# Kernel tuning notes

Hardware: AMD Instinct MI355X
Metric: run time of the kernel (lower is better)

The kernel has to match this reference:

```python
import jax, jax.numpy as jnp
import numpy as np


def setup_inputs() -> dict:
    key = jax.random.key(0)
    k1, k2 = jax.random.split(key)
    qs = jax.random.normal(k1, (8, 4096, 1024), dtype=jnp.float32)      # [B, L, D]
    memory = jax.random.normal(k2, (512, 1024), dtype=jnp.float32)       # [M, D]
    return {"qs": qs, "memory": memory}


def reference(qs, memory):
    # s = qs @ memory.T  -> [B, L, M]; permute -> [B, M, L]
    s = jnp.einsum("bld,md->bml", qs, memory)
    # softmax over L (last dim after permute)
    v = jax.nn.softmax(s, axis=2)                 # [B, M, L]
    # r = v @ qs -> [B, M, D]
    r = jnp.einsum("bml,bld->bmd", v, qs)
    return (r, memory)
```

## Files before the change

### kernel.cpp

```cpp
#include <hip/hip_runtime.h>
#include <hip/hip_fp16.h>


#define B_ 8
#define L_ 4096
#define D_ 1024
#define M_ 512

typedef _Float16 halfT;
typedef _Float16 half8 __attribute__((ext_vector_type(8)));
typedef _Float16 half4_t __attribute__((ext_vector_type(4)));
typedef float f32x4 __attribute__((ext_vector_type(4)));

#define OFF_MEM16 0ull
#define SZ_MEM16  (512ull*1024*2)
#define OFF_QS16  (OFF_MEM16 + SZ_MEM16)
#define SZ_QS16   (8ull*4096*1024*2)
#define OFF_S     (OFF_QS16 + SZ_QS16)
#define SZ_S      (8ull*512*4096*4)
#define OFF_P16   (OFF_S + SZ_S)
#define SZ_P16    (8ull*512*4096*2)
#define OFF_INVL  (OFF_P16 + SZ_P16)
#define SZ_INVL   (8ull*512*4)
#define WS_NEED   (OFF_INVL + SZ_INVL)
#define OFF_RP    OFF_S

#define SWZ(n) ((((n)&7) ^ (((n)>>5)&7)))

__device__ __forceinline__ void gload_lds16(const halfT* g, halfT* l) {
  __builtin_amdgcn_global_load_lds(
      (const __attribute__((address_space(1))) unsigned int*)(const void*)g,
      (__attribute__((address_space(3))) unsigned int*)l, 16, 0, 0);
}

__global__ __launch_bounds__(256)
void prep_mem16(const float* __restrict__ mem, halfT* __restrict__ mem16) {
  int i8 = blockIdx.x*256 + threadIdx.x;
  int row = i8 >> 7, c = i8 & 127;
  int kt = c >> 3, g = c & 7;
  const float* src = mem + (size_t)i8*8;
  f32x4 x0 = *(const f32x4*)src;
  f32x4 x1 = *(const f32x4*)(src + 4);
  half8 h;
  #pragma unroll
  for (int j = 0; j < 4; ++j) { h[j] = (halfT)x0[j]; h[4+j] = (halfT)x1[j]; }
  *(half8*)&mem16[(size_t)row*1024 + kt*64 + ((g ^ (row & 7)) << 3)] = h;
}

__global__ __launch_bounds__(256)
void prep_qs16(const float* __restrict__ qs, halfT* __restrict__ q16) {
  size_t base = (size_t)blockIdx.x*256 + threadIdx.x;
  #pragma unroll
  for (int it = 0; it < 8; ++it) {
    size_t i8 = base + (size_t)it*524288;
    size_t row = i8 >> 7;
    int c = (int)(i8 & 127);
    int kt = c >> 3, g = c & 7;
    const float* src = qs + i8*8;
    f32x4 x0 = *(const f32x4*)src;
    f32x4 x1 = *(const f32x4*)(src + 4);
    half8 h;
    #pragma unroll
    for (int j = 0; j < 4; ++j) { h[j] = (halfT)x0[j]; h[4+j] = (halfT)x1[j]; }
    *(half8*)&q16[row*1024 + kt*64 + ((g ^ ((int)row & 7)) << 3)] = h;
  }
}

__global__ __launch_bounds__(512, 2)
void gemm_qk(const halfT* __restrict__ mem16, const halfT* __restrict__ qs16,
             float* __restrict__ S)
{
  __shared__ __attribute__((aligned(16))) halfT At[2][256*64];
  __shared__ __attribute__((aligned(16))) halfT Bt[2][256*64];

  int bid = blockIdx.x;
  int swz = (bid & 7)*32 + (bid >> 3);
  int b   = swz >> 5;
  int rem = swz & 31;
  int nt  = rem >> 1;
  int mt  = rem & 1;

  int tid = threadIdx.x;
  int w = tid >> 6, lane = tid & 63, lg = lane >> 4, li = lane & 15;
  int wm = w >> 2, wn = w & 3;
  int sl = li & 7;
  int rA = tid >> 3;
  int cA = (tid & 7)*8;

  const halfT* Ab = mem16 + (size_t)mt*256*1024;
  const halfT* Bb = qs16 + ((size_t)b*L_ + nt*256)*D_;

  f32x4 acc[8][4];
  #pragma unroll
  for (int i=0;i<8;++i)
    #pragma unroll
    for (int j=0;j<4;++j) acc[i][j] = (f32x4){0.f,0.f,0.f,0.f};

#define STAGE_QK(nb_, kt_)                                                     \
  do {                                                                         \
    const halfT* a0 = Ab + (size_t)(kt_)*64 + cA;                              \
    const halfT* b0 = Bb + (size_t)(kt_)*64 + cA;                              \
    _Pragma("unroll")                                                          \
    for (int j = 0; j < 4; ++j) {                                              \
      int r = rA + j*64;                                                       \
      gload_lds16(a0 + (size_t)r*1024, &At[nb_][(tid + j*512)*8]);             \
      gload_lds16(b0 + (size_t)r*1024, &Bt[nb_][(tid + j*512)*8]);             \
    }                                                                          \
  } while (0)

  STAGE_QK(0, 0);
  __syncthreads();

  int nb = 0;
  for (int kt = 0; kt < 16; ++kt) {
    if (kt + 1 < 16) STAGE_QK(nb ^ 1, kt + 1);
    #pragma unroll
    for (int ksub = 0; ksub < 2; ++ksub) {
      int gx = ((ksub*4 + lg) ^ sl) << 3;
      half8 Af[8], Bf[4];
      #pragma unroll
      for (int mf = 0; mf < 8; ++mf)
        Af[mf] = *(const half8*)&At[nb][(wm*128 + mf*16 + li)*64 + gx];
      #pragma unroll
      for (int nf = 0; nf < 4; ++nf)
        Bf[nf] = *(const half8*)&Bt[nb][(wn*64 + nf*16 + li)*64 + gx];
      #pragma unroll
      for (int mf = 0; mf < 8; ++mf)
        #pragma unroll
        for (int nf = 0; nf < 4; ++nf)
          acc[mf][nf] = __builtin_amdgcn_mfma_f32_16x16x32_f16(Af[mf], Bf[nf], acc[mf][nf], 0,0,0);
    }
    __syncthreads();
    nb ^= 1;
  }
#undef STAGE_QK

  float* Cb = S + (size_t)b*M_*L_;
  int colbase = nt*256 + wn*64;
  #pragma unroll
  for (int mf = 0; mf < 8; ++mf) {
    #pragma unroll
    for (int r = 0; r < 4; ++r) {
      int row = mt*256 + wm*128 + mf*16 + lg*4 + r;
      #pragma unroll
      for (int nf = 0; nf < 4; ++nf)
        Cb[(size_t)row*L_ + colbase + nf*16 + li] = acc[mf][nf][r];
    }
  }
}

__global__ __launch_bounds__(512, 2)
void gemm_pv(const halfT* __restrict__ P16, const halfT* __restrict__ qs16,
             float* __restrict__ rp)
{
  __shared__ __attribute__((aligned(16))) halfT At[2][256*64];
  __shared__ __attribute__((aligned(16))) halfT Bt[2][256*64];

  int bid = blockIdx.x;
  int swz = (bid & 7)*32 + (bid >> 3);
  int ks  = swz >> 6;
  int rem = swz & 63;
  int b   = rem >> 3;
  int nt  = (rem >> 1) & 3;
  int mt  = rem & 1;

  int tid = threadIdx.x;
  int w = tid >> 6, lane = tid & 63, lg = lane >> 4, li = lane & 15;
  int wm = w >> 2, wn = w & 3;
  int sl = li & 7;

  const halfT* Ab = P16 + (size_t)b*M_*L_ + (size_t)mt*256*L_ + ks*1024;
  const halfT* Bb = qs16 + ((size_t)b*L_ + ks*1024)*D_ + nt*256;
  int krow = tid >> 3;
  int seg  = tid & 7;
  int rs   = krow & 7;

  f32x4 acc[8][4];
  #pragma unroll
  for (int i=0;i<8;++i)
    #pragma unroll
    for (int j=0;j<4;++j) acc[i][j] = (f32x4){0.f,0.f,0.f,0.f};

  half8 hx[4];

#define GLOADB_PV(kt_)                                                         \
  do {                                                                         \
    const halfT* rowp = Bb + (size_t)((kt_)*64 + krow)*D_ + (seg >> 1)*64;     \
    _Pragma("unroll")                                                          \
    for (int j = 0; j < 4; ++j)                                                \
      hx[j] = *(const half8*)(rowp + ((((seg & 1)*4 + j) ^ rs) << 3));         \
  } while (0)

#define STAGEA_PV(nb_, kt_)                                                    \
  do {                                                                         \
    const halfT* a0 = Ab + (size_t)(kt_)*64 + (tid & 7)*8;                     \
    _Pragma("unroll")                                                          \
    for (int j = 0; j < 4; ++j)                                                \
      gload_lds16(a0 + (size_t)((tid >> 3) + j*64)*L_, &At[nb_][(tid + j*512)*8]); \
  } while (0)

#define WRITEB_PV(nb_)                                                         \
  do {                                                                         \
    _Pragma("unroll")                                                          \
    for (int i = 0; i < 32; ++i) {                                             \
      int n_ = seg*32 + i;                                                     \
      Bt[nb_][n_*64 + ((((krow >> 3) ^ SWZ(n_)) << 3)) + (krow & 7)] =         \
          hx[i >> 3][i & 7];                                                   \
    }                                                                          \
  } while (0)

  GLOADB_PV(0);
  STAGEA_PV(0, 0);
  WRITEB_PV(0);
  __syncthreads();

  int nb = 0;
  for (int kt = 0; kt < 16; ++kt) {
    if (kt + 1 < 16) { GLOADB_PV(kt + 1); STAGEA_PV(nb ^ 1, kt + 1); }
    #pragma unroll
    for (int ksub = 0; ksub < 2; ++ksub) {
      int gx = ((ksub*4 + lg) ^ sl) << 3;
      half8 Af[8], Bf[4];
      #pragma unroll
      for (int mf = 0; mf < 8; ++mf)
        Af[mf] = *(const half8*)&At[nb][(wm*128 + mf*16 + li)*64 + gx];
      #pragma unroll
      for (int nf = 0; nf < 4; ++nf) {
        int n_ = wn*64 + nf*16 + li;
        Bf[nf] = *(const half8*)&Bt[nb][n_*64 + (((ksub*4 + lg) ^ SWZ(n_)) << 3)];
      }
      #pragma unroll
      for (int mf = 0; mf < 8; ++mf)
        #pragma unroll
        for (int nf = 0; nf < 4; ++nf)
          acc[mf][nf] = __builtin_amdgcn_mfma_f32_16x16x32_f16(Af[mf], Bf[nf], acc[mf][nf], 0,0,0);
    }
    if (kt + 1 < 16) WRITEB_PV(nb ^ 1);
    __syncthreads();
    nb ^= 1;
  }
#undef GLOADB_PV
#undef STAGEA_PV
#undef WRITEB_PV

  float* Cb = rp + (size_t)ks*((size_t)B_*M_*D_) + (size_t)b*M_*D_;
  int colbase = nt*256 + wn*64;
  #pragma unroll
  for (int mf = 0; mf < 8; ++mf) {
    #pragma unroll
    for (int r = 0; r < 4; ++r) {
      int row = mt*256 + wm*128 + mf*16 + lg*4 + r;
      #pragma unroll
      for (int nf = 0; nf < 4; ++nf)
        Cb[(size_t)row*D_ + colbase + nf*16 + li] = acc[mf][nf][r];
    }
  }
}

__global__ __launch_bounds__(256)
void softmax_rows(const float* __restrict__ S, halfT* __restrict__ P,
                  float* __restrict__ invl)
{
  __shared__ float red[4];
  int row = blockIdx.x;
  int rs  = row & 7;
  int tid = threadIdx.x;
  const float* src = S + (size_t)row*L_;
  f32x4 v[4];
  float mx = -3.0e38f;
  #pragma unroll
  for (int i = 0; i < 4; ++i) {
    v[i] = *(const f32x4*)&src[(size_t)(i*256 + tid)*4];
    #pragma unroll
    for (int e = 0; e < 4; ++e) mx = fmaxf(mx, v[i][e]);
  }
  #pragma unroll
  for (int off = 1; off < 64; off <<= 1) mx = fmaxf(mx, __shfl_xor(mx, off));
  int w = tid >> 6;
  if ((tid & 63) == 0) red[w] = mx;
  __syncthreads();
  mx = fmaxf(fmaxf(red[0], red[1]), fmaxf(red[2], red[3]));

  float sum = 0.f;
  halfT* dst = P + (size_t)row*L_;
  #pragma unroll
  for (int i = 0; i < 4; ++i) {
    half4_t h;
    #pragma unroll
    for (int e = 0; e < 4; ++e) {
      float ev = __expf(v[i][e] - mx);
      sum += ev;
      h[e] = (halfT)ev;
    }
    int idx4 = i*256 + tid;
    int kt = idx4 >> 4, g = (idx4 >> 1) & 7, o = idx4 & 1;
    *(half4_t*)&dst[kt*64 + ((g ^ rs) << 3) + o*4] = h;
  }
  #pragma unroll
  for (int off = 1; off < 64; off <<= 1) sum += __shfl_xor(sum, off);
  __syncthreads();
  if ((tid & 63) == 0) red[w] = sum;
  __syncthreads();
  if (tid == 0) invl[row] = 1.0f / (red[0] + red[1] + red[2] + red[3]);
}

__global__ __launch_bounds__(256)
void combine_scale(const float* __restrict__ rp, const float* __restrict__ invl,
                   float* __restrict__ out)
{
  int bm = blockIdx.x;
  int tid = threadIdx.x;
  size_t off = (size_t)bm*D_ + tid*4;
  f32x4 v = *(const f32x4*)&rp[off];
  #pragma unroll
  for (int s = 1; s < 4; ++s)
    v += *(const f32x4*)&rp[(size_t)s*B_*M_*D_ + off];
  float sc = invl[bm];
  v *= sc;
  *(f32x4*)&out[off] = v;
}

__global__ void fallback_kernel(const float* __restrict__ qs,
                                const float* __restrict__ mem,
                                float* __restrict__ out)
{
  __shared__ float w_lds[4][4096];
  __shared__ float mem_s[4][1024];
  __shared__ float redb[256];
  int blk = blockIdx.x;
  int b = blk >> 7;
  int m0 = (blk & 127)*4;
  int tid = threadIdx.x;

  for (int i = tid; i < 4*1024; i += 256)
    mem_s[i>>10][i&1023] = mem[(size_t)(m0 + (i>>10))*D_ + (i&1023)];
  __syncthreads();

  float mx[4] = {-3e38f,-3e38f,-3e38f,-3e38f};
  for (int l = tid; l < L_; l += 256) {
    const float* qp = qs + ((size_t)b*L_ + l)*D_;
    float dot[4] = {0,0,0,0};
    for (int dd = 0; dd < D_; dd += 4) {
      f32x4 qv = *(const f32x4*)(qp + dd);
      #pragma unroll
      for (int mi=0; mi<4; ++mi)
        dot[mi] += qv[0]*mem_s[mi][dd] + qv[1]*mem_s[mi][dd+1]
                 + qv[2]*mem_s[mi][dd+2] + qv[3]*mem_s[mi][dd+3];
    }
    #pragma unroll
    for (int mi=0; mi<4; ++mi) { w_lds[mi][l] = dot[mi]; mx[mi] = fmaxf(mx[mi], dot[mi]); }
  }
  float Mv[4], Zv[4];
  for (int mi=0; mi<4; ++mi) {
    redb[tid] = mx[mi]; __syncthreads();
    for (int s=128; s>0; s>>=1) { if (tid<s) redb[tid]=fmaxf(redb[tid],redb[tid+s]); __syncthreads(); }
    Mv[mi] = redb[0]; __syncthreads();
  }
  float sm[4] = {0,0,0,0};
  for (int l = tid; l < L_; l += 256)
    #pragma unroll
    for (int mi=0; mi<4; ++mi) {
      float wv = __expf(w_lds[mi][l] - Mv[mi]);
      w_lds[mi][l] = wv; sm[mi] += wv;
    }
  for (int mi=0; mi<4; ++mi) {
    redb[tid] = sm[mi]; __syncthreads();
    for (int s=128; s>0; s>>=1) { if (tid<s) redb[tid]+=redb[tid+s]; __syncthreads(); }
    Zv[mi] = redb[0]; __syncthreads();
  }
  int d0 = tid*4;
  f32x4 a[4];
  #pragma unroll
  for (int mi=0;mi<4;++mi) a[mi] = (f32x4){0,0,0,0};
  for (int l = 0; l < L_; ++l) {
    f32x4 qv = *(const f32x4*)(qs + ((size_t)b*L_ + l)*D_ + d0);
    #pragma unroll
    for (int mi=0; mi<4; ++mi) a[mi] += qv * w_lds[mi][l];
  }
  #pragma unroll
  for (int mi=0; mi<4; ++mi) {
    float invz = 1.f/Zv[mi];
    #pragma unroll
    for (int c=0; c<4; ++c)
      out[((size_t)b*M_ + m0 + mi)*D_ + d0 + c] = a[mi][c]*invz;
  }
}

extern "C" void kernel_launch(void* const* d_in, const int* in_sizes, int n_in,
                              void* d_out, int out_size, void* d_ws, size_t ws_size,
                              hipStream_t stream) {
  const float* qs  = (const float*)d_in[0];
  const float* mem = (const float*)d_in[1];
  float* out = (float*)d_out;

  hipMemcpyAsync(out + (size_t)B_*M_*D_, mem, (size_t)M_*D_*sizeof(float),
                 hipMemcpyDeviceToDevice, stream);

  if (ws_size >= (size_t)WS_NEED) {
    char* base = (char*)d_ws;
    halfT* mem16 = (halfT*)(base + OFF_MEM16);
    halfT* qs16  = (halfT*)(base + OFF_QS16);
    float* S     = (float*)(base + OFF_S);
    halfT* P16   = (halfT*)(base + OFF_P16);
    float* invl  = (float*)(base + OFF_INVL);
    float* rp    = (float*)(base + OFF_RP);

    prep_mem16<<<256, 256, 0, stream>>>(mem, mem16);
    prep_qs16<<<2048, 256, 0, stream>>>(qs, qs16);
    gemm_qk<<<256, 512, 0, stream>>>(mem16, qs16, S);
    softmax_rows<<<4096, 256, 0, stream>>>(S, P16, invl);
    gemm_pv<<<256, 512, 0, stream>>>(P16, qs16, rp);
    combine_scale<<<4096, 256, 0, stream>>>(rp, invl, out);
  } else {
    fallback_kernel<<<1024, 256, 0, stream>>>(qs, mem, out);
  }
}
```

Baseline: 165.6 us.

## Deepen GEMM global-to-LDS prefetch to two stages with explicit vmcnt waits

Both the QK and PV GEMM main loops now issue global-to-LDS loads two k-tiles ahead instead of one. The full __syncthreads drain is replaced by raw s_barrier plus targeted s_waitcnt vmcnt(8), so only the older stage's loads must land before compute. This is meant to hide global memory latency behind a full iteration of MFMA work instead of stalling at each barrier. It relies on hand-counted outstanding load numbers and sched_barriers, which is fragile if the compiler changes how many loads each stage issues.

Result: faster. 158.4 us (-4.3%).

```diff
diff --git a/kernel.cpp b/kernel.cpp
--- a/kernel.cpp
+++ b/kernel.cpp
@@ -108,32 +108,46 @@
     }                                                                          \
   } while (0)
 
+#define COMPUTE_QK(nb_)                                                        \
+  do {                                                                         \
+    _Pragma("unroll")                                                          \
+    for (int ksub = 0; ksub < 2; ++ksub) {                                     \
+      int gx = ((ksub*4 + lg) ^ sl) << 3;                                      \
+      half8 Af[8], Bf[4];                                                      \
+      _Pragma("unroll")                                                        \
+      for (int mf = 0; mf < 8; ++mf)                                           \
+        Af[mf] = *(const half8*)&At[nb_][(wm*128 + mf*16 + li)*64 + gx];       \
+      _Pragma("unroll")                                                        \
+      for (int nf = 0; nf < 4; ++nf)                                           \
+        Bf[nf] = *(const half8*)&Bt[nb_][(wn*64 + nf*16 + li)*64 + gx];        \
+      _Pragma("unroll")                                                        \
+      for (int mf = 0; mf < 8; ++mf)                                           \
+        _Pragma("unroll")                                                      \
+        for (int nf = 0; nf < 4; ++nf)                                         \
+          acc[mf][nf] = __builtin_amdgcn_mfma_f32_16x16x32_f16(Af[mf], Bf[nf], acc[mf][nf], 0,0,0); \
+    }                                                                          \
+  } while (0)
+
   STAGE_QK(0, 0);
-  __syncthreads();
-
-  int nb = 0;
+  STAGE_QK(1, 1);
+  asm volatile("s_waitcnt vmcnt(8)" ::: "memory");
+  __builtin_amdgcn_sched_barrier(0);
+  __builtin_amdgcn_s_barrier();
+
   for (int kt = 0; kt < 16; ++kt) {
-    if (kt + 1 < 16) STAGE_QK(nb ^ 1, kt + 1);
-    #pragma unroll
-    for (int ksub = 0; ksub < 2; ++ksub) {
-      int gx = ((ksub*4 + lg) ^ sl) << 3;
-      half8 Af[8], Bf[4];
-      #pragma unroll
-      for (int mf = 0; mf < 8; ++mf)
-        Af[mf] = *(const half8*)&At[nb][(wm*128 + mf*16 + li)*64 + gx];
-      #pragma unroll
-      for (int nf = 0; nf < 4; ++nf)
-        Bf[nf] = *(const half8*)&Bt[nb][(wn*64 + nf*16 + li)*64 + gx];
-      #pragma unroll
-      for (int mf = 0; mf < 8; ++mf)
-        #pragma unroll
-        for (int nf = 0; nf < 4; ++nf)
-          acc[mf][nf] = __builtin_amdgcn_mfma_f32_16x16x32_f16(Af[mf], Bf[nf], acc[mf][nf], 0,0,0);
-    }
-    __syncthreads();
-    nb ^= 1;
+    COMPUTE_QK(kt & 1);
+    __builtin_amdgcn_s_barrier();
+    if (kt + 2 < 16) {
+      STAGE_QK(kt & 1, kt + 2);
+      asm volatile("s_waitcnt vmcnt(8) lgkmcnt(0)" ::: "memory");
+    } else {
+      asm volatile("s_waitcnt vmcnt(0) lgkmcnt(0)" ::: "memory");
+    }
+    __builtin_amdgcn_sched_barrier(0);
+    __builtin_amdgcn_s_barrier();
   }
 #undef STAGE_QK
+#undef COMPUTE_QK
 
   float* Cb = S + (size_t)b*M_*L_;
   int colbase = nt*256 + wn*64;
@@ -209,39 +223,55 @@
     }                                                                          \
   } while (0)
 
+#define COMPUTE_PV(nb_)                                                        \
+  do {                                                                         \
+    _Pragma("unroll")                                                          \
+    for (int ksub = 0; ksub < 2; ++ksub) {                                     \
+      int gx = ((ksub*4 + lg) ^ sl) << 3;                                      \
+      half8 Af[8], Bf[4];                                                      \
+      _Pragma("unroll")                                                        \
+      for (int mf = 0; mf < 8; ++mf)                                           \
+        Af[mf] = *(const half8*)&At[nb_][(wm*128 + mf*16 + li)*64 + gx];       \
+      _Pragma("unroll")                                                        \
+      for (int nf = 0; nf < 4; ++nf) {                                         \
+        int n_ = wn*64 + nf*16 + li;                                           \
+        Bf[nf] = *(const half8*)&Bt[nb_][n_*64 + (((ksub*4 + lg) ^ SWZ(n_)) << 3)]; \
+      }                                                                        \
+      _Pragma("unroll")                                                        \
+      for (int mf = 0; mf < 8; ++mf)                                           \
+        _Pragma("unroll")                                                      \
+        for (int nf = 0; nf < 4; ++nf)                                         \
+          acc[mf][nf] = __builtin_amdgcn_mfma_f32_16x16x32_f16(Af[mf], Bf[nf], acc[mf][nf], 0,0,0); \
+    }                                                                          \
+  } while (0)
+
   GLOADB_PV(0);
   STAGEA_PV(0, 0);
+  STAGEA_PV(1, 1);
   WRITEB_PV(0);
-  __syncthreads();
-
-  int nb = 0;
+  GLOADB_PV(1);
+  asm volatile("s_waitcnt vmcnt(8) lgkmcnt(0)" ::: "memory");
+  __builtin_amdgcn_sched_barrier(0);
+  __builtin_amdgcn_s_barrier();
+
   for (int kt = 0; kt < 16; ++kt) {
-    if (kt + 1 < 16) { GLOADB_PV(kt + 1); STAGEA_PV(nb ^ 1, kt + 1); }
-    #pragma unroll
-    for (int ksub = 0; ksub < 2; ++ksub) {
-      int gx = ((ksub*4 + lg) ^ sl) << 3;
-      half8 Af[8], Bf[4];
-      #pragma unroll
-      for (int mf = 0; mf < 8; ++mf)
-        Af[mf] = *(const half8*)&At[nb][(wm*128 + mf*16 + li)*64 + gx];
-      #pragma unroll
-      for (int nf = 0; nf < 4; ++nf) {
-        int n_ = wn*64 + nf*16 + li;
-        Bf[nf] = *(const half8*)&Bt[nb][n_*64 + (((ksub*4 + lg) ^ SWZ(n_)) << 3)];
-      }
-      #pragma unroll
-      for (int mf = 0; mf < 8; ++mf)
-        #pragma unroll
-        for (int nf = 0; nf < 4; ++nf)
-          acc[mf][nf] = __builtin_amdgcn_mfma_f32_16x16x32_f16(Af[mf], Bf[nf], acc[mf][nf], 0,0,0);
-    }
-    if (kt + 1 < 16) WRITEB_PV(nb ^ 1);
-    __syncthreads();
-    nb ^= 1;
+    COMPUTE_PV(kt & 1);
+    __builtin_amdgcn_s_barrier();
+    if (kt + 1 < 16) WRITEB_PV((kt + 1) & 1);
+    if (kt + 2 < 16) {
+      GLOADB_PV(kt + 2);
+      STAGEA_PV(kt & 1, kt + 2);
+      asm volatile("s_waitcnt vmcnt(8) lgkmcnt(0)" ::: "memory");
+    } else {
+      asm volatile("s_waitcnt vmcnt(0) lgkmcnt(0)" ::: "memory");
+    }
+    __builtin_amdgcn_sched_barrier(0);
+    __builtin_amdgcn_s_barrier();
   }
 #undef GLOADB_PV
 #undef STAGEA_PV
 #undef WRITEB_PV
+#undef COMPUTE_PV
 
   float* Cb = rp + (size_t)ks*((size_t)B_*M_*D_) + (size_t)b*M_*D_;
   int colbase = nt*256 + wn*64;
```
